# Optimization experiments

Measured on AMD Instinct MI355X. Metric: run time of the kernel, lower is better.

The kernel has to match this reference:

```python
import jax, jax.numpy as jnp
import numpy as np

NUM_LAYERS = 6
D_MODEL = 768
N_HEADS = 8
D_QKV = D_MODEL // N_HEADS
D_FF = 3072
OUT_DIM = 80
MAX_REL = 100  # relative_positional_distance
NUM_REL = 2 * MAX_REL + 1
LN_EPS = 1e-5


def layer_norm(x, g, b):
    mu = jnp.mean(x, axis=-1, keepdims=True)
    var = jnp.mean((x - mu) ** 2, axis=-1, keepdims=True)
    return (x - mu) / jnp.sqrt(var + LN_EPS) * g + b


def rel_positional_logits(q, emb):
    # q: (B,H,L,dq) (already scaled by 1/sqrt(dq)); emb: (H, 2*MAX_REL+1, dq)
    B, H, L, dq = q.shape
    pad_len = max(L - MAX_REL, 0)
    start = max(MAX_REL - L, 0)
    padded = jnp.pad(emb, ((0, 0), (pad_len, pad_len), (0, 0)))
    used = padded[:, start:start + 2 * L - 1]  # (H, 2L-1, dq)
    logits = jnp.einsum('bhld,hmd->bhlm', q, used)  # (B,H,L,2L-1)
    if L > MAX_REL:
        # mask unreachable relative positions (|rel| beyond table) with -1e8
        mask = jnp.zeros((2 * L - 1,), logits.dtype)
        mask = mask.at[:pad_len].set(-1e8).at[-pad_len:].set(-1e8)
        logits = logits + mask
    # relative -> absolute indexing (fairseq skew trick)
    x = jnp.pad(logits, ((0, 0), (0, 0), (0, 0), (0, 1)))       # (B,H,L,2L)
    x = x.reshape(B, H, L * 2 * L)
    x = jnp.pad(x, ((0, 0), (0, 0), (0, L - 1)))
    x = x.reshape(B, H, L + 1, 2 * L - 1)
    return x[:, :, :L, L - 1:]  # (B,H,L,L)


def self_attention(x, wq, wk, wv, wo, emb):
    # x: (T,B,D); wq/wk/wv: (H,D,dq); wo: (H,dq,D); emb: (H,NUM_REL,dq)
    q = jnp.einsum('tbf,hfa->bhta', x, wq) / (D_QKV ** 0.5)
    k = jnp.einsum('tbf,hfa->bhta', x, wk)
    v = jnp.einsum('tbf,hfa->bhta', x, wv)
    logits = jnp.einsum('bhqa,bhka->bhqk', q, k) + rel_positional_logits(q, emb)
    probs = jax.nn.softmax(logits, axis=-1)
    o = jnp.einsum('bhqk,bhka->bhqa', probs, v)
    return jnp.einsum('bhta,had->tbd', o, wo)


def forward(x, wq, wk, wv, wo, rel_emb, ff1_w, ff1_b, ff2_w, ff2_b,
            ln1_g, ln1_b, ln2_g, ln2_b, wout, bout):
    # x: (B,T,D)
    src = jnp.transpose(x, (1, 0, 2))  # (T,B,D)
    for l in range(NUM_LAYERS):
        attn = self_attention(src, wq[l], wk[l], wv[l], wo[l], rel_emb[l])
        src = layer_norm(src + attn, ln1_g[l], ln1_b[l])
        h = jax.nn.relu(src @ ff1_w[l].T + ff1_b[l])
        ff = h @ ff2_w[l].T + ff2_b[l]
        src = layer_norm(src + ff, ln2_g[l], ln2_b[l])
    out = jnp.transpose(src, (1, 0, 2))  # (B,T,D)
    return out @ wout.T + bout


def setup_inputs() -> dict:
    key = jax.random.key(0)
    ks = jax.random.split(key, 17)
    B, T = 8, 512
    s_d = 1.0 / np.sqrt(D_MODEL)
    s_q = 1.0 / np.sqrt(D_QKV)
    s_f = 1.0 / np.sqrt(D_FF)
    f32 = jnp.float32
    return {
        'x': jax.random.normal(ks[0], (B, T, D_MODEL), f32),
        'wq': jax.random.normal(ks[1], (NUM_LAYERS, N_HEADS, D_MODEL, D_QKV), f32) * s_d,
        'wk': jax.random.normal(ks[2], (NUM_LAYERS, N_HEADS, D_MODEL, D_QKV), f32) * s_d,
        'wv': jax.random.normal(ks[3], (NUM_LAYERS, N_HEADS, D_MODEL, D_QKV), f32) * s_d,
        'wo': jax.random.normal(ks[4], (NUM_LAYERS, N_HEADS, D_QKV, D_MODEL), f32) * s_q,
        'rel_emb': jax.random.normal(ks[5], (NUM_LAYERS, N_HEADS, NUM_REL, D_QKV), f32) * s_q,
        'ff1_w': jax.random.normal(ks[6], (NUM_LAYERS, D_FF, D_MODEL), f32) * s_d,
        'ff1_b': jnp.zeros((NUM_LAYERS, D_FF), f32),
        'ff2_w': jax.random.normal(ks[7], (NUM_LAYERS, D_MODEL, D_FF), f32) * s_f,
        'ff2_b': jnp.zeros((NUM_LAYERS, D_MODEL), f32),
        'ln1_g': jnp.ones((NUM_LAYERS, D_MODEL), f32),
        'ln1_b': jnp.zeros((NUM_LAYERS, D_MODEL), f32),
        'ln2_g': jnp.ones((NUM_LAYERS, D_MODEL), f32),
        'ln2_b': jnp.zeros((NUM_LAYERS, D_MODEL), f32),
        'wout': jax.random.normal(ks[8], (OUT_DIM, D_MODEL), f32) * s_d,
        'bout': jnp.zeros((OUT_DIM,), f32),
    }


def reference(x, wq, wk, wv, wo, rel_emb, ff1_w, ff1_b, ff2_w, ff2_b,
              ln1_g, ln1_b, ln2_g, ln2_b, wout, bout):
    return forward(x, wq, wk, wv, wo, rel_emb, ff1_w, ff1_b, ff2_w, ff2_b,
                   ln1_g, ln1_b, ln2_g, ln2_b, wout, bout)
```

## Files before the change

kernel.cpp:

```cpp
#include <hip/hip_runtime.h>
#include <hip/hip_bf16.h>
#include <math.h>

#define NL   6
#define DM   768
#define NH   8
#define DQ   96
#define DFF  3072
#define BB   8
#define TT   512
#define NTOK (BB*TT)
#define NREL 201
#define WIN  99
#define ODIM 80
#define NQKV 2304
#define RELD 208

typedef __attribute__((ext_vector_type(8))) short v8s;
typedef __attribute__((ext_vector_type(4))) float v4f;

static __device__ __forceinline__ short bf16bits(float x) {
  __hip_bfloat16 h = __float2bfloat16(x);
  return *(short*)&h;
}

__global__ void k_transpose_in(const float* __restrict__ x, float* __restrict__ src,
                               __hip_bfloat16* __restrict__ srcb) {
  int n = blockIdx.x;
  int t = n >> 3, b = n & 7;
  const float* xi = x + ((size_t)b*TT + t)*DM;
  for (int d = threadIdx.x; d < DM; d += blockDim.x) {
    float v = xi[d];
    src[(size_t)n*DM + d] = v;
    srcb[(size_t)n*DM + d] = __float2bfloat16(v);
  }
}

__global__ void k_conv_qkvw(const float* __restrict__ wq, const float* __restrict__ wk,
                            const float* __restrict__ wv, __hip_bfloat16* __restrict__ o) {
  int idx = blockIdx.x*256 + threadIdx.x;
  if (idx >= NQKV*DM) return;
  int f = idx % DM, n = idx / DM;
  int part = n / DM, c = n % DM;
  int h = c / DQ, a = c % DQ;
  size_t si = ((size_t)h*DM + f)*DQ + a;
  float v = (part == 0) ? wq[si]*0.10206207261596577f : (part == 1 ? wk[si] : wv[si]);
  o[idx] = __float2bfloat16(v);
}

__global__ void k_conv_wo(const float* __restrict__ wo, __hip_bfloat16* __restrict__ o) {
  int idx = blockIdx.x*256 + threadIdx.x;
  if (idx >= DM*DM) return;
  int r = idx % DM, d = idx / DM;
  o[idx] = __float2bfloat16(wo[(size_t)r*DM + d]);
}

__global__ void k_cast(const float* __restrict__ in, __hip_bfloat16* __restrict__ o, int n) {
  int idx = blockIdx.x*256 + threadIdx.x;
  if (idx < n) o[idx] = __float2bfloat16(in[idx]);
}

__global__ void k_conv_wout(const float* __restrict__ wout, __hip_bfloat16* __restrict__ o) {
  int idx = blockIdx.x*256 + threadIdx.x;
  if (idx >= 128*DM) return;
  int n = idx / DM, f = idx % DM;
  o[idx] = __float2bfloat16(n < ODIM ? wout[(size_t)n*DM + f] : 0.f);
}

template<int BM, int BN, int WM, int WN, bool RELU, bool BF16OUT, bool PERM>
__global__ __launch_bounds__(256)
void k_mfma_gemm(const __hip_bfloat16* __restrict__ A, const __hip_bfloat16* __restrict__ Bt,
                 const float* __restrict__ bias, void* __restrict__ Cv,
                 int K, int Nvalid, int ldc) {
  constexpr int NWN = BN/WN;
  constexpr int FM = WM/16, FN = WN/16;
  __shared__ __align__(16) short As[BM*64];
  __shared__ __align__(16) short Bs[BN*64];
  const int tid = threadIdx.x;
  const int m0 = blockIdx.y*BM, n0 = blockIdx.x*BN;
  const int lane = tid & 63, w = tid >> 6;
  const int wm = (w / NWN)*WM, wn = (w % NWN)*WN;
  const int mr = lane & 15, q4 = lane >> 4;
  const short* Ag = (const short*)A;
  const short* Bg = (const short*)Bt;
  const v4f zero = {0.f, 0.f, 0.f, 0.f};
  v4f acc[FM][FN];
  #pragma unroll
  for (int i=0;i<FM;++i)
    #pragma unroll
    for (int j=0;j<FN;++j) acc[i][j] = zero;

  for (int k0 = 0; k0 < K; k0 += 64) {
    #pragma unroll
    for (int s = 0; s < (BM*8)/256; ++s) {
      int cid = s*256 + tid;
      int row = cid >> 3;
      int c = (cid & 7) ^ (row & 7);
      __builtin_amdgcn_global_load_lds(
        (const __attribute__((address_space(1))) void*)(Ag + (size_t)(m0+row)*K + k0 + c*8),
        (__attribute__((address_space(3))) void*)(As + cid*8), 16, 0, 0);
    }
    #pragma unroll
    for (int s = 0; s < (BN*8)/256; ++s) {
      int cid = s*256 + tid;
      int row = cid >> 3;
      int c = (cid & 7) ^ (row & 7);
      __builtin_amdgcn_global_load_lds(
        (const __attribute__((address_space(1))) void*)(Bg + (size_t)(n0+row)*K + k0 + c*8),
        (__attribute__((address_space(3))) void*)(Bs + cid*8), 16, 0, 0);
    }
    __syncthreads();
    #pragma unroll
    for (int kh = 0; kh < 2; ++kh) {
      int pos = (kh*4 + q4) ^ (mr & 7);
      v8s af[FM], bf[FN];
      #pragma unroll
      for (int i=0;i<FM;++i) af[i] = *(const v8s*)(As + (wm + i*16 + mr)*64 + pos*8);
      #pragma unroll
      for (int j=0;j<FN;++j) bf[j] = *(const v8s*)(Bs + (wn + j*16 + mr)*64 + pos*8);
      #pragma unroll
      for (int i=0;i<FM;++i)
        #pragma unroll
        for (int j=0;j<FN;++j)
          acc[i][j] = __builtin_amdgcn_mfma_f32_16x16x32_bf16(af[i], bf[j], acc[i][j], 0, 0, 0);
    }
    __syncthreads();
  }

  #pragma unroll
  for (int j=0;j<FN;++j) {
    int col = n0 + wn + j*16 + mr;
    if (col < Nvalid) {
      float bv = bias ? bias[col] : 0.f;
      #pragma unroll
      for (int i=0;i<FM;++i) {
        #pragma unroll
        for (int r=0;r<4;++r) {
          int m = m0 + wm + i*16 + q4*4 + r;
          float val = acc[i][j][r] + bv;
          if (RELU) val = fmaxf(val, 0.f);
          int row = PERM ? ((m & 7)*TT + (m >> 3)) : m;
          if (BF16OUT) ((__hip_bfloat16*)Cv)[(size_t)row*ldc + col] = __float2bfloat16(val);
          else         ((float*)Cv)[(size_t)row*ldc + col] = val;
        }
      }
    }
  }
}

__global__ __launch_bounds__(256)
void k_rel_gemm(const __hip_bfloat16* __restrict__ qkvb,
                const __hip_bfloat16* __restrict__ embb,
                float* __restrict__ rel) {
  const int e0 = blockIdx.x*64, m0 = blockIdx.y*64, h = blockIdx.z;
  const int tid = threadIdx.x, lane = tid & 63, w = tid >> 6;
  const int l15 = lane & 15, q4 = lane >> 4;
  __shared__ __align__(16) short As[64*104];
  __shared__ __align__(16) short Bs[64*104];
  const short* qg = (const short*)qkvb;
  const short* eg = (const short*)embb;
  {
    int row = tid >> 2;
    const short* sa = qg + (size_t)(m0+row)*NQKV + h*DQ;
    int er = e0 + row; if (er > 200) er = 200;
    const short* sb = eg + ((size_t)h*NREL + er)*DQ;
    short* da = As + row*104;
    short* db = Bs + row*104;
    #pragma unroll
    for (int c = 0; c < 3; ++c) {
      int ch = (tid & 3)*3 + c;
      *(v8s*)(da + ch*8) = *(const v8s*)(sa + ch*8);
      *(v8s*)(db + ch*8) = *(const v8s*)(sb + ch*8);
    }
  }
  __syncthreads();
  const v4f zero = {0.f,0.f,0.f,0.f};
  v4f acc[4] = {zero, zero, zero, zero};
  #pragma unroll
  for (int ks = 0; ks < 3; ++ks) {
    v8s af = *(const v8s*)(As + (w*16 + l15)*104 + ks*32 + q4*8);
    #pragma unroll
    for (int f = 0; f < 4; ++f) {
      v8s bf = *(const v8s*)(Bs + (f*16 + l15)*104 + ks*32 + q4*8);
      acc[f] = __builtin_amdgcn_mfma_f32_16x16x32_bf16(af, bf, acc[f], 0, 0, 0);
    }
  }
  #pragma unroll
  for (int f = 0; f < 4; ++f) {
    int e = e0 + f*16 + l15;
    if (e < 2*WIN + 1) {
      #pragma unroll
      for (int r = 0; r < 4; ++r) {
        int n = m0 + w*16 + q4*4 + r;
        rel[((size_t)h*NTOK + n)*RELD + e] = acc[f][r];
      }
    }
  }
}

__global__ __launch_bounds__(256)
void k_attn_mfma(const __hip_bfloat16* __restrict__ qkvb,
                 const float* __restrict__ rel,
                 __hip_bfloat16* __restrict__ o) {
  const int qt = blockIdx.x, h = blockIdx.y, b = blockIdx.z;
  const int qlo = qt*64;
  const int tid = threadIdx.x, lane = tid & 63, w = tid >> 6;
  const int l15 = lane & 15, q4 = lane >> 4;
  __shared__ __align__(16) short Qs[64*104];
  __shared__ __align__(16) short Ks[64*104];
  __shared__ __align__(16) short Vt[96*72];
  __shared__ __align__(16) short Ps[64*72];
  const short* qg = (const short*)qkvb;

  {
    int row = tid >> 2;
    const short* src = qg + (size_t)((qlo+row)*8 + b)*NQKV + h*DQ;
    short* dst = Qs + row*104;
    #pragma unroll
    for (int c = 0; c < 3; ++c) {
      int ch = (tid & 3)*3 + c;
      *(v8s*)(dst + ch*8) = *(const v8s*)(src + ch*8);
    }
  }

  v4f sacc[5][4];
  const v4f neg = {-1e30f,-1e30f,-1e30f,-1e30f};
  #pragma unroll
  for (int kt=0;kt<5;++kt)
    #pragma unroll
    for (int f=0;f<4;++f) sacc[kt][f] = neg;

  const int i_row0 = qlo + w*16 + q4*4;

  for (int kt = 0; kt < 5; ++kt) {
    int kt0 = qlo + kt*64 - 128;
    if (kt0 + 64 <= 0 || kt0 >= TT) continue;
    {
      int row = tid >> 2;
      int j = kt0 + row; j = j < 0 ? 0 : (j > TT-1 ? TT-1 : j);
      const short* src = qg + (size_t)(j*8 + b)*NQKV + DM + h*DQ;
      short* dst = Ks + row*104;
      #pragma unroll
      for (int c = 0; c < 3; ++c) {
        int ch = (tid & 3)*3 + c;
        *(v8s*)(dst + ch*8) = *(const v8s*)(src + ch*8);
      }
    }
    __syncthreads();
    #pragma unroll
    for (int f = 0; f < 4; ++f) {
      int j = kt0 + f*16 + l15;
      #pragma unroll
      for (int r = 0; r < 4; ++r) {
        int i = i_row0 + r;
        int d = j - i;
        float val = -1e30f;
        if (j >= 0 && j < TT && d >= -WIN && d <= WIN)
          val = rel[((size_t)h*NTOK + i*8 + b)*RELD + d + WIN];
        sacc[kt][f][r] = val;
      }
    }
    #pragma unroll
    for (int ks = 0; ks < 3; ++ks) {
      v8s af = *(const v8s*)(Qs + (w*16 + l15)*104 + ks*32 + q4*8);
      #pragma unroll
      for (int f = 0; f < 4; ++f) {
        v8s bf = *(const v8s*)(Ks + (f*16 + l15)*104 + ks*32 + q4*8);
        sacc[kt][f] = __builtin_amdgcn_mfma_f32_16x16x32_bf16(af, bf, sacc[kt][f], 0, 0, 0);
      }
    }
    __syncthreads();
  }

  float inv[4];
  #pragma unroll
  for (int r = 0; r < 4; ++r) {
    float m = -1e30f;
    #pragma unroll
    for (int kt=0;kt<5;++kt)
      #pragma unroll
      for (int f=0;f<4;++f) m = fmaxf(m, sacc[kt][f][r]);
    #pragma unroll
    for (int off=1; off<16; off<<=1) m = fmaxf(m, __shfl_xor(m, off));
    float l = 0.f;
    #pragma unroll
    for (int kt=0;kt<5;++kt)
      #pragma unroll
      for (int f=0;f<4;++f) {
        float p = __expf(sacc[kt][f][r] - m);
        sacc[kt][f][r] = p; l += p;
      }
    #pragma unroll
    for (int off=1; off<16; off<<=1) l += __shfl_xor(l, off);
    inv[r] = 1.f / l;
  }

  v4f oacc[6];
  const v4f zero = {0.f,0.f,0.f,0.f};
  #pragma unroll
  for (int f=0;f<6;++f) oacc[f] = zero;
  for (int kt = 0; kt < 5; ++kt) {
    int kt0 = qlo + kt*64 - 128;
    if (kt0 + 64 <= 0 || kt0 >= TT) continue;
    #pragma unroll
    for (int f=0;f<4;++f)
      #pragma unroll
      for (int r=0;r<4;++r)
        Ps[(w*16 + q4*4 + r)*72 + f*16 + l15] = bf16bits(sacc[kt][f][r]);
    {
      int j = kt0 + (tid >> 2);
      int jc = j < 0 ? 0 : (j > TT-1 ? TT-1 : j);
      const short* src = qg + (size_t)(jc*8 + b)*NQKV + 2*DM + h*DQ + (tid & 3)*24;
      union { v8s v[3]; short s[24]; } u;
      u.v[0] = *(const v8s*)(src);
      u.v[1] = *(const v8s*)(src + 8);
      u.v[2] = *(const v8s*)(src + 16);
      int a0 = (tid & 3)*24, jl = tid >> 2;
      #pragma unroll
      for (int t=0;t<24;++t) Vt[(a0+t)*72 + jl] = u.s[t];
    }
    __syncthreads();
    #pragma unroll
    for (int ks=0;ks<2;++ks) {
      v8s af = *(const v8s*)(Ps + (w*16 + l15)*72 + ks*32 + q4*8);
      #pragma unroll
      for (int f=0;f<6;++f) {
        v8s bf = *(const v8s*)(Vt + (f*16 + l15)*72 + ks*32 + q4*8);
        oacc[f] = __builtin_amdgcn_mfma_f32_16x16x32_bf16(af, bf, oacc[f], 0, 0, 0);
      }
    }
    __syncthreads();
  }

  #pragma unroll
  for (int f=0;f<6;++f)
    #pragma unroll
    for (int r=0;r<4;++r) {
      int i = i_row0 + r;
      o[(size_t)(i*8 + b)*DM + h*DQ + f*16 + l15] = __float2bfloat16(oacc[f][r] * inv[r]);
    }
}

__global__ __launch_bounds__(256)
void k_ln_residual(float* __restrict__ src, const float* __restrict__ res,
                   const float* __restrict__ g, const float* __restrict__ bta,
                   __hip_bfloat16* __restrict__ srcb) {
  __shared__ float red[4];
  int n = blockIdx.x;
  float x[3];
  float s = 0.f;
  #pragma unroll
  for (int u=0;u<3;++u) {
    int d = u*256 + threadIdx.x;
    x[u] = src[(size_t)n*DM + d] + res[(size_t)n*DM + d];
    s += x[u];
  }
  #pragma unroll
  for (int off=32; off; off>>=1) s += __shfl_xor(s, off);
  if ((threadIdx.x & 63) == 0) red[threadIdx.x>>6] = s;
  __syncthreads();
  float mu = (red[0]+red[1]+red[2]+red[3]) * (1.f/DM);
  __syncthreads();
  float vs = 0.f;
  #pragma unroll
  for (int u=0;u<3;++u) { float dv = x[u]-mu; vs += dv*dv; }
  #pragma unroll
  for (int off=32; off; off>>=1) vs += __shfl_xor(vs, off);
  if ((threadIdx.x & 63) == 0) red[threadIdx.x>>6] = vs;
  __syncthreads();
  float rstd = rsqrtf((red[0]+red[1]+red[2]+red[3])*(1.f/DM) + 1e-5f);
  #pragma unroll
  for (int u=0;u<3;++u) {
    int d = u*256 + threadIdx.x;
    float v = (x[u]-mu)*rstd*g[d] + bta[d];
    src[(size_t)n*DM + d] = v;
    srcb[(size_t)n*DM + d] = __float2bfloat16(v);
  }
}

extern "C" void kernel_launch(void* const* d_in, const int* in_sizes, int n_in,
                              void* d_out, int out_size, void* d_ws, size_t ws_size,
                              hipStream_t stream) {
  const float* x    = (const float*)d_in[0];
  const float* wq   = (const float*)d_in[1];
  const float* wk   = (const float*)d_in[2];
  const float* wv   = (const float*)d_in[3];
  const float* wo   = (const float*)d_in[4];
  const float* remb = (const float*)d_in[5];
  const float* ff1w = (const float*)d_in[6];
  const float* ff1b = (const float*)d_in[7];
  const float* ff2w = (const float*)d_in[8];
  const float* ff2b = (const float*)d_in[9];
  const float* ln1g = (const float*)d_in[10];
  const float* ln1b = (const float*)d_in[11];
  const float* ln2g = (const float*)d_in[12];
  const float* ln2b = (const float*)d_in[13];
  const float* wout = (const float*)d_in[14];
  const float* bout = (const float*)d_in[15];
  float* out = (float*)d_out;

  float* wsp = (float*)d_ws;
  size_t off = 0;
  float* src  = wsp + off;                              off += (size_t)NTOK*DM;
  __hip_bfloat16* srcb  = (__hip_bfloat16*)(wsp + off); off += (size_t)NTOK*DM/2;
  __hip_bfloat16* qkvb  = (__hip_bfloat16*)(wsp + off); off += (size_t)NTOK*NQKV/2;
  float* rel  = wsp + off;                              off += (size_t)NH*NTOK*RELD;
  float* tmp  = wsp + off;                              off += (size_t)NTOK*DM;
  __hip_bfloat16* qkvwb = (__hip_bfloat16*)(wsp + off); off += (size_t)NQKV*DM/2;
  __hip_bfloat16* wob   = (__hip_bfloat16*)(wsp + off); off += (size_t)DM*DM/2;
  __hip_bfloat16* ff1wb = (__hip_bfloat16*)(wsp + off); off += (size_t)DFF*DM/2;
  __hip_bfloat16* ff2wb = (__hip_bfloat16*)(wsp + off); off += (size_t)DM*DFF/2;
  __hip_bfloat16* woutb = (__hip_bfloat16*)(wsp + off); off += (size_t)128*DM/2;
  __hip_bfloat16* embb  = (__hip_bfloat16*)(wsp + off); off += (size_t)NH*NREL*DQ/2 + 64;
  __hip_bfloat16* hb  = (__hip_bfloat16*)qkvb;
  __hip_bfloat16* obb = srcb;
  (void)off; (void)ws_size; (void)in_sizes; (void)n_in; (void)out_size;

  dim3 b256(256);

  k_transpose_in<<<dim3(NTOK), b256, 0, stream>>>(x, src, srcb);

  for (int l = 0; l < NL; ++l) {
    k_conv_qkvw<<<dim3((NQKV*DM+255)/256), b256, 0, stream>>>(
        wq + (size_t)l*DM*DM, wk + (size_t)l*DM*DM, wv + (size_t)l*DM*DM, qkvwb);
    k_conv_wo<<<dim3((DM*DM+255)/256), b256, 0, stream>>>(wo + (size_t)l*DM*DM, wob);
    k_cast<<<dim3((DFF*DM+255)/256), b256, 0, stream>>>(ff1w + (size_t)l*DFF*DM, ff1wb, DFF*DM);
    k_cast<<<dim3((DM*DFF+255)/256), b256, 0, stream>>>(ff2w + (size_t)l*DM*DFF, ff2wb, DM*DFF);
    k_cast<<<dim3((NH*NREL*DQ+255)/256), b256, 0, stream>>>(remb + (size_t)l*NH*NREL*DQ,
                                                            embb, NH*NREL*DQ);

    k_mfma_gemm<128,128,64,64,false,true,false><<<dim3(NQKV/128, NTOK/128), b256, 0, stream>>>(
        srcb, qkvwb, nullptr, qkvb, DM, NQKV, NQKV);

    k_rel_gemm<<<dim3(4, NTOK/64, NH), b256, 0, stream>>>(qkvb, embb, rel);

    k_attn_mfma<<<dim3(TT/64, NH, BB), b256, 0, stream>>>(qkvb, rel, obb);

    k_mfma_gemm<64,128,64,32,false,false,false><<<dim3(DM/128, NTOK/64), b256, 0, stream>>>(
        obb, wob, nullptr, tmp, DM, DM, DM);
    k_ln_residual<<<dim3(NTOK), b256, 0, stream>>>(src, tmp, ln1g + (size_t)l*DM, ln1b + (size_t)l*DM, srcb);

    k_mfma_gemm<128,128,64,64,true,true,false><<<dim3(DFF/128, NTOK/128), b256, 0, stream>>>(
        srcb, ff1wb, ff1b + (size_t)l*DFF, hb, DM, DFF, DFF);
    k_mfma_gemm<64,128,64,32,false,false,false><<<dim3(DM/128, NTOK/64), b256, 0, stream>>>(
        hb, ff2wb, ff2b + (size_t)l*DM, tmp, DFF, DM, DM);
    k_ln_residual<<<dim3(NTOK), b256, 0, stream>>>(src, tmp, ln2g + (size_t)l*DM, ln2b + (size_t)l*DM, srcb);
  }

  k_conv_wout<<<dim3((128*DM+255)/256), b256, 0, stream>>>(wout, woutb);
  k_mfma_gemm<64,128,64,32,false,false,true><<<dim3(1, NTOK/64), b256, 0, stream>>>(
      srcb, woutb, bout, out, DM, ODIM, ODIM);
}
```

Baseline: 1.339 ms.

## Double-buffer GEMM LDS, batch weight conversion, retile GEMMs and swap grid axes

The GEMM kernel now keeps two LDS buffers, so it issues the next K-tile's global-to-LDS loads before computing on the current one, with one barrier per iteration. All per-layer weight conversion launches are replaced by single launches that convert every layer's weights up front into larger workspace arrays. GEMM tile shapes are reduced (64x128 for QKV/FF1, 64x64 for the output projection and FF2), and the grid mapping is swapped so blockIdx.x walks M. The smaller tiles raise block counts and the batched conversion removes launch overhead, at the cost of more workspace and less reuse per tile.

```diff
diff --git a/kernel.cpp b/kernel.cpp
--- a/kernel.cpp
+++ b/kernel.cpp
@@ -38,25 +38,27 @@
 
 __global__ void k_conv_qkvw(const float* __restrict__ wq, const float* __restrict__ wk,
                             const float* __restrict__ wv, __hip_bfloat16* __restrict__ o) {
-  int idx = blockIdx.x*256 + threadIdx.x;
-  if (idx >= NQKV*DM) return;
-  int f = idx % DM, n = idx / DM;
+  size_t idx = (size_t)blockIdx.x*256 + threadIdx.x;
+  if (idx >= (size_t)NL*NQKV*DM) return;
+  int f = idx % DM; size_t rest = idx / DM;
+  int n = rest % NQKV; int l = rest / NQKV;
   int part = n / DM, c = n % DM;
   int h = c / DQ, a = c % DQ;
-  size_t si = ((size_t)h*DM + f)*DQ + a;
+  size_t si = (size_t)l*DM*DM + ((size_t)h*DM + f)*DQ + a;
   float v = (part == 0) ? wq[si]*0.10206207261596577f : (part == 1 ? wk[si] : wv[si]);
   o[idx] = __float2bfloat16(v);
 }
 
 __global__ void k_conv_wo(const float* __restrict__ wo, __hip_bfloat16* __restrict__ o) {
-  int idx = blockIdx.x*256 + threadIdx.x;
-  if (idx >= DM*DM) return;
-  int r = idx % DM, d = idx / DM;
-  o[idx] = __float2bfloat16(wo[(size_t)r*DM + d]);
-}
-
-__global__ void k_cast(const float* __restrict__ in, __hip_bfloat16* __restrict__ o, int n) {
-  int idx = blockIdx.x*256 + threadIdx.x;
+  size_t idx = (size_t)blockIdx.x*256 + threadIdx.x;
+  if (idx >= (size_t)NL*DM*DM) return;
+  int r = idx % DM; size_t rest = idx / DM;
+  int d = rest % DM; int l = rest / DM;
+  o[idx] = __float2bfloat16(wo[(size_t)l*DM*DM + (size_t)r*DM + d]);
+}
+
+__global__ void k_cast(const float* __restrict__ in, __hip_bfloat16* __restrict__ o, size_t n) {
+  size_t idx = (size_t)blockIdx.x*256 + threadIdx.x;
   if (idx < n) o[idx] = __float2bfloat16(in[idx]);
 }
 
@@ -74,10 +76,10 @@
                  int K, int Nvalid, int ldc) {
   constexpr int NWN = BN/WN;
   constexpr int FM = WM/16, FN = WN/16;
-  __shared__ __align__(16) short As[BM*64];
-  __shared__ __align__(16) short Bs[BN*64];
+  __shared__ __align__(16) short As[2][BM*64];
+  __shared__ __align__(16) short Bs[2][BN*64];
   const int tid = threadIdx.x;
-  const int m0 = blockIdx.y*BM, n0 = blockIdx.x*BN;
+  const int m0 = blockIdx.x*BM, n0 = blockIdx.y*BN;
   const int lane = tid & 63, w = tid >> 6;
   const int wm = (w / NWN)*WM, wn = (w % NWN)*WN;
   const int mr = lane & 15, q4 = lane >> 4;
@@ -90,7 +92,7 @@
     #pragma unroll
     for (int j=0;j<FN;++j) acc[i][j] = zero;
 
-  for (int k0 = 0; k0 < K; k0 += 64) {
+  auto stage = [&](int k0, int buf) {
     #pragma unroll
     for (int s = 0; s < (BM*8)/256; ++s) {
       int cid = s*256 + tid;
@@ -98,7 +100,7 @@
       int c = (cid & 7) ^ (row & 7);
       __builtin_amdgcn_global_load_lds(
         (const __attribute__((address_space(1))) void*)(Ag + (size_t)(m0+row)*K + k0 + c*8),
-        (__attribute__((address_space(3))) void*)(As + cid*8), 16, 0, 0);
+        (__attribute__((address_space(3))) void*)(&As[buf][cid*8]), 16, 0, 0);
     }
     #pragma unroll
     for (int s = 0; s < (BN*8)/256; ++s) {
@@ -107,24 +109,31 @@
       int c = (cid & 7) ^ (row & 7);
       __builtin_amdgcn_global_load_lds(
         (const __attribute__((address_space(1))) void*)(Bg + (size_t)(n0+row)*K + k0 + c*8),
-        (__attribute__((address_space(3))) void*)(Bs + cid*8), 16, 0, 0);
-    }
+        (__attribute__((address_space(3))) void*)(&Bs[buf][cid*8]), 16, 0, 0);
+    }
+  };
+
+  const int nk = K >> 6;
+  stage(0, 0);
+  for (int i = 0; i < nk; ++i) {
     __syncthreads();
+    if (i + 1 < nk) stage((i+1)*64, (i+1)&1);
+    const short* Ab = As[i&1];
+    const short* Bb = Bs[i&1];
     #pragma unroll
     for (int kh = 0; kh < 2; ++kh) {
       int pos = (kh*4 + q4) ^ (mr & 7);
       v8s af[FM], bf[FN];
       #pragma unroll
-      for (int i=0;i<FM;++i) af[i] = *(const v8s*)(As + (wm + i*16 + mr)*64 + pos*8);
-      #pragma unroll
-      for (int j=0;j<FN;++j) bf[j] = *(const v8s*)(Bs + (wn + j*16 + mr)*64 + pos*8);
-      #pragma unroll
-      for (int i=0;i<FM;++i)
+      for (int ii=0;ii<FM;++ii) af[ii] = *(const v8s*)(Ab + (wm + ii*16 + mr)*64 + pos*8);
+      #pragma unroll
+      for (int j=0;j<FN;++j) bf[j] = *(const v8s*)(Bb + (wn + j*16 + mr)*64 + pos*8);
+      #pragma unroll
+      for (int ii=0;ii<FM;++ii)
         #pragma unroll
         for (int j=0;j<FN;++j)
-          acc[i][j] = __builtin_amdgcn_mfma_f32_16x16x32_bf16(af[i], bf[j], acc[i][j], 0, 0, 0);
-    }
-    __syncthreads();
+          acc[ii][j] = __builtin_amdgcn_mfma_f32_16x16x32_bf16(af[ii], bf[j], acc[ii][j], 0, 0, 0);
+    }
   }
 
   #pragma unroll
@@ -406,48 +415,52 @@
   __hip_bfloat16* qkvb  = (__hip_bfloat16*)(wsp + off); off += (size_t)NTOK*NQKV/2;
   float* rel  = wsp + off;                              off += (size_t)NH*NTOK*RELD;
   float* tmp  = wsp + off;                              off += (size_t)NTOK*DM;
-  __hip_bfloat16* qkvwb = (__hip_bfloat16*)(wsp + off); off += (size_t)NQKV*DM/2;
-  __hip_bfloat16* wob   = (__hip_bfloat16*)(wsp + off); off += (size_t)DM*DM/2;
-  __hip_bfloat16* ff1wb = (__hip_bfloat16*)(wsp + off); off += (size_t)DFF*DM/2;
-  __hip_bfloat16* ff2wb = (__hip_bfloat16*)(wsp + off); off += (size_t)DM*DFF/2;
-  __hip_bfloat16* woutb = (__hip_bfloat16*)(wsp + off); off += (size_t)128*DM/2;
-  __hip_bfloat16* embb  = (__hip_bfloat16*)(wsp + off); off += (size_t)NH*NREL*DQ/2 + 64;
+  __hip_bfloat16* qkvwbA = (__hip_bfloat16*)(wsp + off); off += (size_t)NL*NQKV*DM/2;
+  __hip_bfloat16* wobA   = (__hip_bfloat16*)(wsp + off); off += (size_t)NL*DM*DM/2;
+  __hip_bfloat16* ff1wbA = (__hip_bfloat16*)(wsp + off); off += (size_t)NL*DFF*DM/2;
+  __hip_bfloat16* ff2wbA = (__hip_bfloat16*)(wsp + off); off += (size_t)NL*DM*DFF/2;
+  __hip_bfloat16* woutb  = (__hip_bfloat16*)(wsp + off); off += (size_t)128*DM/2;
+  __hip_bfloat16* embbA  = (__hip_bfloat16*)(wsp + off); off += (size_t)NL*NH*NREL*DQ/2 + 64;
   __hip_bfloat16* hb  = (__hip_bfloat16*)qkvb;
   __hip_bfloat16* obb = srcb;
   (void)off; (void)ws_size; (void)in_sizes; (void)n_in; (void)out_size;
 
   dim3 b256(256);
 
+  k_conv_qkvw<<<dim3(((size_t)NL*NQKV*DM+255)/256), b256, 0, stream>>>(wq, wk, wv, qkvwbA);
+  k_conv_wo<<<dim3(((size_t)NL*DM*DM+255)/256), b256, 0, stream>>>(wo, wobA);
+  k_cast<<<dim3(((size_t)NL*DFF*DM+255)/256), b256, 0, stream>>>(ff1w, ff1wbA, (size_t)NL*DFF*DM);
+  k_cast<<<dim3(((size_t)NL*DM*DFF+255)/256), b256, 0, stream>>>(ff2w, ff2wbA, (size_t)NL*DM*DFF);
+  k_cast<<<dim3(((size_t)NL*NH*NREL*DQ+255)/256), b256, 0, stream>>>(remb, embbA, (size_t)NL*NH*NREL*DQ);
+  k_conv_wout<<<dim3((128*DM+255)/256), b256, 0, stream>>>(wout, woutb);
+
   k_transpose_in<<<dim3(NTOK), b256, 0, stream>>>(x, src, srcb);
 
   for (int l = 0; l < NL; ++l) {
-    k_conv_qkvw<<<dim3((NQKV*DM+255)/256), b256, 0, stream>>>(
-        wq + (size_t)l*DM*DM, wk + (size_t)l*DM*DM, wv + (size_t)l*DM*DM, qkvwb);
-    k_conv_wo<<<dim3((DM*DM+255)/256), b256, 0, stream>>>(wo + (size_t)l*DM*DM, wob);
-    k_cast<<<dim3((DFF*DM+255)/256), b256, 0, stream>>>(ff1w + (size_t)l*DFF*DM, ff1wb, DFF*DM);
-    k_cast<<<dim3((DM*DFF+255)/256), b256, 0, stream>>>(ff2w + (size_t)l*DM*DFF, ff2wb, DM*DFF);
-    k_cast<<<dim3((NH*NREL*DQ+255)/256), b256, 0, stream>>>(remb + (size_t)l*NH*NREL*DQ,
-                                                            embb, NH*NREL*DQ);
-
-    k_mfma_gemm<128,128,64,64,false,true,false><<<dim3(NQKV/128, NTOK/128), b256, 0, stream>>>(
+    __hip_bfloat16* qkvwb = qkvwbA + (size_t)l*NQKV*DM;
+    __hip_bfloat16* wob   = wobA   + (size_t)l*DM*DM;
+    __hip_bfloat16* ff1wb = ff1wbA + (size_t)l*DFF*DM;
+    __hip_bfloat16* ff2wb = ff2wbA + (size_t)l*DM*DFF;
+    __hip_bfloat16* embb  = embbA  + (size_t)l*NH*NREL*DQ;
+
+    k_mfma_gemm<64,128,64,32,false,true,false><<<dim3(NTOK/64, NQKV/128), b256, 0, stream>>>(
         srcb, qkvwb, nullptr, qkvb, DM, NQKV, NQKV);
 
     k_rel_gemm<<<dim3(4, NTOK/64, NH), b256, 0, stream>>>(qkvb, embb, rel);
 
     k_attn_mfma<<<dim3(TT/64, NH, BB), b256, 0, stream>>>(qkvb, rel, obb);
 
-    k_mfma_gemm<64,128,64,32,false,false,false><<<dim3(DM/128, NTOK/64), b256, 0, stream>>>(
+    k_mfma_gemm<64,64,32,32,false,false,false><<<dim3(NTOK/64, DM/64), b256, 0, stream>>>(
         obb, wob, nullptr, tmp, DM, DM, DM);
     k_ln_residual<<<dim3(NTOK), b256, 0, stream>>>(src, tmp, ln1g + (size_t)l*DM, ln1b + (size_t)l*DM, srcb);
 
-    k_mfma_gemm<128,128,64,64,true,true,false><<<dim3(DFF/128, NTOK/128), b256, 0, stream>>>(
+    k_mfma_gemm<64,128,64,32,true,true,false><<<dim3(NTOK/64, DFF/128), b256, 0, stream>>>(
         srcb, ff1wb, ff1b + (size_t)l*DFF, hb, DM, DFF, DFF);
-    k_mfma_gemm<64,128,64,32,false,false,false><<<dim3(DM/128, NTOK/64), b256, 0, stream>>>(
+    k_mfma_gemm<64,64,32,32,false,false,false><<<dim3(NTOK/64, DM/64), b256, 0, stream>>>(
         hb, ff2wb, ff2b + (size_t)l*DM, tmp, DFF, DM, DM);
     k_ln_residual<<<dim3(NTOK), b256, 0, stream>>>(src, tmp, ln2g + (size_t)l*DM, ln2b + (size_t)l*DM, srcb);
   }
 
-  k_conv_wout<<<dim3((128*DM+255)/256), b256, 0, stream>>>(wout, woutb);
-  k_mfma_gemm<64,128,64,32,false,false,true><<<dim3(1, NTOK/64), b256, 0, stream>>>(
+  k_mfma_gemm<64,128,64,32,false,false,true><<<dim3(NTOK/64, 1), b256, 0, stream>>>(
       srcb, woutb, bout, out, DM, ODIM, ODIM);
 }
```

Result: faster. 1.305 ms (-2.5%).
